# Kernel optimization log

Hardware: AMD Instinct MI355X
Metric: run time of the kernel (lower is better)

## Reference

```python
import jax, jax.numpy as jnp
import numpy as np

S, D, H, MLP = 2048, 1024, 16, 4096
DK = D // H
EPS = 1e-5  # torch LayerNorm default


def setup_inputs() -> dict:
    key = jax.random.key(0)
    ks = jax.random.split(key, 8)
    init = lambda k, shape, fan_in: jax.random.normal(k, shape, jnp.float32) * (fan_in ** -0.5)
    return {
        "x": jax.random.normal(ks[0], (S, D), jnp.float32),
        "wq": init(ks[1], (D, D), D), "bq": jnp.zeros((D,), jnp.float32),
        "wk": init(ks[2], (D, D), D), "bk": jnp.zeros((D,), jnp.float32),
        "wv": init(ks[3], (D, D), D), "bv": jnp.zeros((D,), jnp.float32),
        "wo": init(ks[4], (D, D), D), "bo": jnp.zeros((D,), jnp.float32),
        "w1": init(ks[5], (D, MLP), D), "b1": jnp.zeros((MLP,), jnp.float32),
        "w2": init(ks[6], (MLP, D), MLP), "b2": jnp.zeros((D,), jnp.float32),
        "ln1_g": jnp.ones((D,), jnp.float32), "ln1_b": jnp.zeros((D,), jnp.float32),
        "ln2_g": jnp.ones((D,), jnp.float32), "ln2_b": jnp.zeros((D,), jnp.float32),
    }


def _layernorm(x, g, b):
    m = jnp.mean(x, axis=-1, keepdims=True)
    v = jnp.var(x, axis=-1, keepdims=True)
    return (x - m) * jax.lax.rsqrt(v + EPS) * g + b


def reference(x, wq, bq, wk, bk, wv, bv, wo, bo, w1, b1, w2, b2, ln1_g, ln1_b, ln2_g, ln2_b):
    # --- residual 1: pre-LN multi-head self-attention ---
    h = _layernorm(x, ln1_g, ln1_b)
    q = (h @ wq + bq).reshape(S, H, DK).transpose(1, 0, 2)  # [H,S,DK]
    k = (h @ wk + bk).reshape(S, H, DK).transpose(1, 0, 2)
    v = (h @ wv + bv).reshape(S, H, DK).transpose(1, 0, 2)
    scores = jnp.einsum('hqd,hkd->hqk', q, k) / jnp.sqrt(jnp.float32(DK))  # [H,S,S]
    attn = jax.nn.softmax(scores, axis=-1)
    o = jnp.einsum('hqk,hkd->hqd', attn, v)  # [H,S,DK]
    # Faithful to original: x.contiguous().view(S, -1) is a raw reshape of the
    # [H,S,DK] buffer (no transpose back to [S,H,DK]).
    o = o.reshape(S, D)
    x = x + (o @ wo + bo)
    # --- residual 2: pre-LN GELU FFN ---
    h2 = _layernorm(x, ln2_g, ln2_b)
    f = jax.nn.gelu(h2 @ w1 + b1, approximate=False)  # torch nn.GELU = exact erf
    x = x + (f @ w2 + b2)
    return x
```

## Files before the change

### kernel.cpp

```cpp
#include <hip/hip_runtime.h>


constexpr int kS = 2048, kD = 1024, kH = 16, kDK = 64, kMLP = 4096;
constexpr float kEps = 1e-5f;

using u16 = unsigned short;
using u32 = unsigned int;
typedef float f32x4 __attribute__((ext_vector_type(4)));
typedef short bf16x8 __attribute__((ext_vector_type(8)));

__device__ __forceinline__ u16 f2b(float f) {
  u32 u = __builtin_bit_cast(u32, f);
  return (u16)((u + 0x7fffu + ((u >> 16) & 1u)) >> 16);
}

typedef const __attribute__((address_space(1))) u32* gas1;
typedef __attribute__((address_space(3))) u32* las3;
__device__ __forceinline__ void async16(const void* g, void* l) {
  __builtin_amdgcn_global_load_lds((gas1)g, (las3)l, 16, 0, 0);
}

__global__ __launch_bounds__(256)
void ln_kernel(const float* __restrict__ x, const float* __restrict__ g,
               const float* __restrict__ b, u16* __restrict__ out) {
  __shared__ float red[8];
  const int row = blockIdx.x, tid = threadIdx.x;
  const float4 v = *(const float4*)(x + (size_t)row * kD + tid * 4);
  float s = v.x + v.y + v.z + v.w;
  float ss = v.x * v.x + v.y * v.y + v.z * v.z + v.w * v.w;
#pragma unroll
  for (int d = 1; d < 64; d <<= 1) { s += __shfl_xor(s, d); ss += __shfl_xor(ss, d); }
  if ((tid & 63) == 0) { red[tid >> 6] = s; red[4 + (tid >> 6)] = ss; }
  __syncthreads();
  const float m = (red[0] + red[1] + red[2] + red[3]) * (1.f / kD);
  const float var = (red[4] + red[5] + red[6] + red[7]) * (1.f / kD) - m * m;
  const float r = rsqrtf(var + kEps);
  const float4 gv = *(const float4*)(g + tid * 4);
  const float4 bv = *(const float4*)(b + tid * 4);
  ushort4 o;
  o.x = f2b((v.x - m) * r * gv.x + bv.x);
  o.y = f2b((v.y - m) * r * gv.y + bv.y);
  o.z = f2b((v.z - m) * r * gv.z + bv.z);
  o.w = f2b((v.w - m) * r * gv.w + bv.w);
  *(ushort4*)(out + (size_t)row * kD + tid * 4) = o;
}

__global__ __launch_bounds__(256)
void transpose_cvt(const float* __restrict__ in, u16* __restrict__ out, int R, int C) {
  __shared__ float tile[32][33];
  const int c0 = blockIdx.x * 32, r0 = blockIdx.y * 32;
  const int x = threadIdx.x, y = threadIdx.y;
#pragma unroll
  for (int i = 0; i < 4; ++i)
    tile[y + i * 8][x] = in[(size_t)(r0 + y + i * 8) * C + c0 + x];
  __syncthreads();
#pragma unroll
  for (int i = 0; i < 4; ++i)
    out[(size_t)(c0 + y + i * 8) * R + r0 + x] = f2b(tile[x][y + i * 8]);
}

__global__ void concat_bias(const float* __restrict__ bq, const float* __restrict__ bk,
                            const float* __restrict__ bv, float* __restrict__ out) {
  int i = blockIdx.x * 256 + threadIdx.x;
  out[i] = i < kD ? bq[i] : (i < 2 * kD ? bk[i - kD] : bv[i - 2 * kD]);
}

__global__ __launch_bounds__(256)
void vtrans(const u16* __restrict__ qkv, u16* __restrict__ vt) {
  __shared__ u16 t[64][72];
  const int s0 = blockIdx.x * 64, h = blockIdx.y, tid = threadIdx.x;
#pragma unroll
  for (int r = 0; r < 2; ++r) {
    int chunk = r * 256 + tid, row = chunk >> 3, col = (chunk & 7) * 8;
    uint4 v = *(const uint4*)(qkv + (size_t)(s0 + row) * 3072 + 2 * kD + h * 64 + col);
    *(uint4*)(&t[row][col]) = v;
  }
  __syncthreads();
#pragma unroll
  for (int r = 0; r < 2; ++r) {
    int chunk = r * 256 + tid, drow = chunk >> 3, scol = (chunk & 7) * 8;
    u16 tmp[8];
#pragma unroll
    for (int j = 0; j < 8; ++j) tmp[j] = t[scol + j][drow];
    *(uint4*)(vt + (size_t)h * 64 * kS + (size_t)drow * kS + s0 + scol) = *(uint4*)tmp;
  }
}

template <int EPI>
__global__ __launch_bounds__(256, 2)
void gemm_bt(const u16* __restrict__ A, const u16* __restrict__ Bt,
             const float* __restrict__ bias, void* __restrict__ Cout,
             int N, int K, int Ksub) {
  constexpr int BM = 128, BN = 128, BK = 32;
  constexpr int MT = 4, NT = 4;
  __shared__ u16 As[BM * BK];
  __shared__ u16 Bs[BN * BK];
  const int tid = threadIdx.x;
  const int w = tid >> 6, l = tid & 63;
  const int wm = w >> 1, wn = w & 1;
  const int row0 = blockIdx.y * BM, col0 = blockIdx.x * BN;
  const int koff = blockIdx.z * Ksub;

  const int sc = ((l & 3) ^ ((l >> 3) & 3)) * 8;
  const u16* Ag = A + (size_t)(row0 + w * 16 + (l >> 2)) * K + koff + sc;
  const u16* Bg = Bt + (size_t)(col0 + w * 16 + (l >> 2)) * K + koff + sc;
  u16* AsW = As + w * 512;
  u16* BsW = Bs + w * 512;

  f32x4 acc[MT][NT] = {};
  const int q = l >> 4;

  for (int kt = 0; kt < Ksub; kt += BK) {
#pragma unroll
    for (int r = 0; r < 2; ++r) async16(Ag + (size_t)r * 64 * K + kt, AsW + r * 2048);
#pragma unroll
    for (int r = 0; r < 2; ++r) async16(Bg + (size_t)r * 64 * K + kt, BsW + r * 2048);
    __syncthreads();
    bf16x8 af[MT], bfr[NT];
#pragma unroll
    for (int i = 0; i < MT; ++i) {
      const int ra = wm * 64 + i * 16 + (l & 15);
      af[i] = *(const bf16x8*)(As + ra * 32 + (q ^ ((ra >> 1) & 3)) * 8);
    }
#pragma unroll
    for (int j = 0; j < NT; ++j) {
      const int rb = wn * 64 + j * 16 + (l & 15);
      bfr[j] = *(const bf16x8*)(Bs + rb * 32 + (q ^ ((rb >> 1) & 3)) * 8);
    }
#pragma unroll
    for (int i = 0; i < MT; ++i)
#pragma unroll
      for (int j = 0; j < NT; ++j)
        acc[i][j] = __builtin_amdgcn_mfma_f32_16x16x32_bf16(af[i], bfr[j], acc[i][j], 0, 0, 0);
    __syncthreads();
  }

  float* Pf = nullptr;
  if constexpr (EPI == 3)
    Pf = (float*)Cout + (size_t)blockIdx.z * gridDim.y * BM * N;
#pragma unroll
  for (int i = 0; i < MT; ++i) {
    const int row = row0 + wm * 64 + i * 16 + ((l >> 4) << 2);
#pragma unroll
    for (int j = 0; j < NT; ++j) {
      const int col = col0 + wn * 64 + j * 16 + (l & 15);
      float bb = 0.f;
      if constexpr (EPI != 3) bb = bias[col];
#pragma unroll
      for (int r = 0; r < 4; ++r) {
        const size_t idx = (size_t)(row + r) * N + col;
        float v = acc[i][j][r] + bb;
        if constexpr (EPI == 0) {
          ((u16*)Cout)[idx] = f2b(v);
        } else if constexpr (EPI == 1) {
          ((u16*)Cout)[idx] = f2b(0.5f * v * (1.f + erff(v * 0.7071067811865475f)));
        } else {
          Pf[idx] = v;
        }
      }
    }
  }
}

template <int KS>
__global__ __launch_bounds__(256)
void reduce_add(const float* __restrict__ parts, const float* __restrict__ bias,
                const float* __restrict__ res, float* __restrict__ out,
                int N, size_t strideMN) {
  const size_t b = ((size_t)blockIdx.x * 256 + threadIdx.x) * 4;
  float4 a = *(const float4*)(res + b);
  const float4 bv = *(const float4*)(bias + (b & (size_t)(N - 1)));
  a.x += bv.x; a.y += bv.y; a.z += bv.z; a.w += bv.w;
#pragma unroll
  for (int s = 0; s < KS; ++s) {
    const float4 p = *(const float4*)(parts + s * strideMN + b);
    a.x += p.x; a.y += p.y; a.z += p.z; a.w += p.w;
  }
  *(float4*)(out + b) = a;
}

__global__ __launch_bounds__(256)
void flash_attn(const u16* __restrict__ qkv, const u16* __restrict__ vt,
                float* __restrict__ Op, float* __restrict__ Ml) {
  constexpr int LP = 140;
  __shared__ u16 PsQ[4 * 16 * LP];
  __shared__ u16 Ks[128 * 64];
  __shared__ u16 Vs[64 * 128];
  const int tid = threadIdx.x, w = tid >> 6, l = tid & 63;
  const int h = blockIdx.y, q0 = blockIdx.x * 64, z = blockIdx.z;
  const int kt0 = z * (kS / 2);
  const int q = l >> 4;

  const u16* Qg = qkv + h * 64;
  const u16* Kg = qkv + kD + h * 64;
  const u16* Vg = vt + (size_t)h * 64 * kS;

  {
    const int r8 = l >> 3, c = (l & 7) ^ r8;
#pragma unroll
    for (int p = 0; p < 2; ++p) {
      const int row = (p * 4 + w) * 8 + r8;
      async16(Qg + (size_t)(q0 + row) * 3072 + c * 8, PsQ + (p * 4 + w) * 512);
    }
  }
  __syncthreads();
  bf16x8 qa[2];
  const int rq = w * 16 + (l & 15);
#pragma unroll
  for (int kq = 0; kq < 2; ++kq)
    qa[kq] = *(const bf16x8*)(PsQ + rq * 64 + ((kq * 4 + q) ^ (l & 7)) * 8);
  u16* Ps = PsQ + w * 16 * LP;

  f32x4 oacc[4] = {};
  float mi[4], li[4];
#pragma unroll
  for (int r = 0; r < 4; ++r) { mi[r] = -1e30f; li[r] = 0.f; }

  for (int it = 0; it < 8; ++it) {
    __syncthreads();
    const int kt = kt0 + it * 128;
    {
      const int r8 = l >> 3, c = (l & 7) ^ r8;
#pragma unroll
      for (int p = 0; p < 4; ++p) {
        const int row = (p * 4 + w) * 8 + r8;
        async16(Kg + (size_t)(kt + row) * 3072 + c * 8, Ks + (p * 4 + w) * 512);
      }
    }
    {
#pragma unroll
      for (int p = 0; p < 4; ++p) {
        const int row = (p * 4 + w) * 4 + (l >> 4);
        const int c = (l & 15) ^ (row & 7);
        async16(Vg + (size_t)row * kS + kt + c * 8, Vs + (p * 4 + w) * 512);
      }
    }
    __syncthreads();

    f32x4 s[8];
#pragma unroll
    for (int n = 0; n < 8; ++n) {
      const int rk = n * 16 + (l & 15);
      f32x4 zz = {};
      bf16x8 kb0 = *(const bf16x8*)(Ks + rk * 64 + ((0 + q) ^ (rk & 7)) * 8);
      bf16x8 kb1 = *(const bf16x8*)(Ks + rk * 64 + ((4 + q) ^ (rk & 7)) * 8);
      zz = __builtin_amdgcn_mfma_f32_16x16x32_bf16(qa[0], kb0, zz, 0, 0, 0);
      zz = __builtin_amdgcn_mfma_f32_16x16x32_bf16(qa[1], kb1, zz, 0, 0, 0);
      s[n] = zz;
    }
    float alpha[4];
#pragma unroll
    for (int r = 0; r < 4; ++r) {
      float m = -1e30f;
#pragma unroll
      for (int n = 0; n < 8; ++n) m = fmaxf(m, s[n][r]);
#pragma unroll
      for (int d = 1; d < 16; d <<= 1) m = fmaxf(m, __shfl_xor(m, d));
      m *= 0.125f;
      float mn = fmaxf(mi[r], m);
      alpha[r] = __expf(mi[r] - mn);
      mi[r] = mn;
      li[r] *= alpha[r];
    }
#pragma unroll
    for (int n = 0; n < 4; ++n)
#pragma unroll
      for (int r = 0; r < 4; ++r) oacc[n][r] *= alpha[r];
    float rs[4] = {0.f, 0.f, 0.f, 0.f};
#pragma unroll
    for (int n = 0; n < 8; ++n)
#pragma unroll
      for (int r = 0; r < 4; ++r) {
        float pv = __expf(s[n][r] * 0.125f - mi[r]);
        rs[r] += pv;
        Ps[((l >> 4) * 4 + r) * LP + n * 16 + (l & 15)] = f2b(pv);
      }
#pragma unroll
    for (int r = 0; r < 4; ++r) {
      float t = rs[r];
#pragma unroll
      for (int d = 1; d < 16; d <<= 1) t += __shfl_xor(t, d);
      li[r] += t;
    }
    bf16x8 pa[4];
#pragma unroll
    for (int ks = 0; ks < 4; ++ks)
      pa[ks] = *(const bf16x8*)(&Ps[(l & 15) * LP + ks * 32 + q * 8]);
#pragma unroll
    for (int n = 0; n < 4; ++n) {
      const int rv = n * 16 + (l & 15);
#pragma unroll
      for (int ks = 0; ks < 4; ++ks) {
        bf16x8 vb = *(const bf16x8*)(Vs + rv * 128 + ((ks * 4 + q) ^ (rv & 7)) * 8);
        oacc[n] = __builtin_amdgcn_mfma_f32_16x16x32_bf16(pa[ks], vb, oacc[n], 0, 0, 0);
      }
    }
  }

#pragma unroll
  for (int r = 0; r < 4; ++r) {
    const int srow = q0 + w * 16 + (l >> 4) * 4 + r;
    const size_t rowIdx = (size_t)(z * kH + h) * kS + srow;
    if ((l & 15) == 0) { Ml[rowIdx * 2] = mi[r]; Ml[rowIdx * 2 + 1] = li[r]; }
#pragma unroll
    for (int n = 0; n < 4; ++n)
      Op[rowIdx * kDK + n * 16 + (l & 15)] = oacc[n][r];
  }
}

__global__ __launch_bounds__(256)
void flash_combine(const float* __restrict__ Op, const float* __restrict__ Ml,
                   u16* __restrict__ og) {
  constexpr size_t HS = (size_t)kH * kS;
  constexpr size_t ZO = HS * kDK;
  const int t = blockIdx.x * 256 + threadIdx.x;
  const int d4 = (t & 15) * 4;
  const size_t row = (size_t)(t >> 4);
  const float m0 = Ml[row * 2], l0 = Ml[row * 2 + 1];
  const float m1 = Ml[(HS + row) * 2], l1 = Ml[(HS + row) * 2 + 1];
  const float m = fmaxf(m0, m1);
  const float w0 = __expf(m0 - m), w1 = __expf(m1 - m);
  const float inv = 1.f / (w0 * l0 + w1 * l1);
  const float4 a = *(const float4*)(Op + row * kDK + d4);
  const float4 b = *(const float4*)(Op + ZO + row * kDK + d4);
  ushort4 o;
  o.x = f2b((w0 * a.x + w1 * b.x) * inv);
  o.y = f2b((w0 * a.y + w1 * b.y) * inv);
  o.z = f2b((w0 * a.z + w1 * b.z) * inv);
  o.w = f2b((w0 * a.w + w1 * b.w) * inv);
  *(ushort4*)(og + row * kDK + d4) = o;
}

extern "C" void kernel_launch(void* const* d_in, const int* in_sizes, int n_in,
                              void* d_out, int out_size, void* d_ws, size_t ws_size,
                              hipStream_t stream) {
  const float* x = (const float*)d_in[0];
  const float* wq = (const float*)d_in[1];
  const float* bq = (const float*)d_in[2];
  const float* wk = (const float*)d_in[3];
  const float* bk = (const float*)d_in[4];
  const float* wv = (const float*)d_in[5];
  const float* bv = (const float*)d_in[6];
  const float* wo = (const float*)d_in[7];
  const float* bo = (const float*)d_in[8];
  const float* w1 = (const float*)d_in[9];
  const float* b1 = (const float*)d_in[10];
  const float* w2 = (const float*)d_in[11];
  const float* b2 = (const float*)d_in[12];
  const float* ln1g = (const float*)d_in[13];
  const float* ln1b = (const float*)d_in[14];
  const float* ln2g = (const float*)d_in[15];
  const float* ln2b = (const float*)d_in[16];
  float* out = (float*)d_out;

  char* p = (char*)d_ws;
  auto alloc = [&](size_t bytes) { void* q = (void*)p; p += (bytes + 255) & ~(size_t)255; return q; };
  u16* h1 = (u16*)alloc((size_t)kS * kD * 2);
  u16* wqkvt = (u16*)alloc((size_t)3 * kD * kD * 2);
  u16* qkv = (u16*)alloc((size_t)kS * 3 * kD * 2);
  u16* vt = (u16*)alloc((size_t)kH * kDK * kS * 2);
  u16* og = (u16*)alloc((size_t)kS * kD * 2);
  u16* wot = (u16*)alloc((size_t)kD * kD * 2);
  u16* h2 = (u16*)alloc((size_t)kS * kD * 2);
  u16* w1t = (u16*)alloc((size_t)kD * kMLP * 2);
  float* bqkv = (float*)alloc((size_t)3 * kD * 4);
  float* x2 = (float*)alloc((size_t)kS * kD * 4);
  u16* fbuf = (u16*)alloc((size_t)kS * kMLP * 2);
  u16* w2t = (u16*)alloc((size_t)kMLP * kD * 2);
  float* part = (float*)d_ws;
  float* Op = x2;
  float* Ml = Op + (size_t)2 * kH * kS * kDK;
  const size_t strideMN = (size_t)kS * kD;

  dim3 tb(32, 8);
  transpose_cvt<<<dim3(kD / 32, kD / 32), tb, 0, stream>>>(wq, wqkvt, kD, kD);
  transpose_cvt<<<dim3(kD / 32, kD / 32), tb, 0, stream>>>(wk, wqkvt + kD * kD, kD, kD);
  transpose_cvt<<<dim3(kD / 32, kD / 32), tb, 0, stream>>>(wv, wqkvt + 2 * kD * kD, kD, kD);
  transpose_cvt<<<dim3(kD / 32, kD / 32), tb, 0, stream>>>(wo, wot, kD, kD);
  transpose_cvt<<<dim3(kMLP / 32, kD / 32), tb, 0, stream>>>(w1, w1t, kD, kMLP);
  transpose_cvt<<<dim3(kD / 32, kMLP / 32), tb, 0, stream>>>(w2, w2t, kMLP, kD);
  concat_bias<<<dim3(12), dim3(256), 0, stream>>>(bq, bk, bv, bqkv);

  ln_kernel<<<dim3(kS), dim3(256), 0, stream>>>(x, ln1g, ln1b, h1);
  gemm_bt<0><<<dim3(3 * kD / 128, kS / 128, 1), dim3(256), 0, stream>>>(
      h1, wqkvt, bqkv, qkv, 3 * kD, kD, kD);
  vtrans<<<dim3(kS / 64, kH), dim3(256), 0, stream>>>(qkv, vt);
  flash_attn<<<dim3(kS / 64, kH, 2), dim3(256), 0, stream>>>(qkv, vt, Op, Ml);
  flash_combine<<<dim3(kH * kS * 16 / 256), dim3(256), 0, stream>>>(Op, Ml, og);
  gemm_bt<3><<<dim3(kD / 128, kS / 128, 2), dim3(256), 0, stream>>>(
      og, wot, nullptr, part, kD, kD, kD / 2);
  reduce_add<2><<<dim3(kS * kD / 4 / 256), dim3(256), 0, stream>>>(
      part, bo, x, x2, kD, strideMN);
  ln_kernel<<<dim3(kS), dim3(256), 0, stream>>>(x2, ln2g, ln2b, h2);
  gemm_bt<1><<<dim3(kMLP / 128, kS / 128, 1), dim3(256), 0, stream>>>(
      h2, w1t, b1, fbuf, kMLP, kD, kD);
  gemm_bt<3><<<dim3(kD / 128, kS / 128, 4), dim3(256), 0, stream>>>(
      fbuf, w2t, nullptr, part, kD, kMLP, kMLP / 4);
  reduce_add<4><<<dim3(kS * kD / 4 / 256), dim3(256), 0, stream>>>(
      part, b2, x2, out, kD, strideMN);
}
```

Baseline: 332.2 us.

## Replace LDS-staged GEMM with direct global-to-register double-buffered MFMA loads

```diff
diff --git a/kernel.cpp b/kernel.cpp
--- a/kernel.cpp
+++ b/kernel.cpp
@@ -87,63 +87,71 @@
 }
 
 template <int EPI>
-__global__ __launch_bounds__(256, 2)
-void gemm_bt(const u16* __restrict__ A, const u16* __restrict__ Bt,
+__global__ __launch_bounds__(256)
+void gemm_rd(const u16* __restrict__ A, const u16* __restrict__ Bt,
              const float* __restrict__ bias, void* __restrict__ Cout,
              int N, int K, int Ksub) {
-  constexpr int BM = 128, BN = 128, BK = 32;
-  constexpr int MT = 4, NT = 4;
-  __shared__ u16 As[BM * BK];
-  __shared__ u16 Bs[BN * BK];
-  const int tid = threadIdx.x;
-  const int w = tid >> 6, l = tid & 63;
+  const int tid = threadIdx.x, w = tid >> 6, l = tid & 63;
   const int wm = w >> 1, wn = w & 1;
-  const int row0 = blockIdx.y * BM, col0 = blockIdx.x * BN;
+  const int row0 = blockIdx.y * 128 + wm * 64;
+  const int col0 = blockIdx.x * 128 + wn * 64;
   const int koff = blockIdx.z * Ksub;
 
-  const int sc = ((l & 3) ^ ((l >> 3) & 3)) * 8;
-  const u16* Ag = A + (size_t)(row0 + w * 16 + (l >> 2)) * K + koff + sc;
-  const u16* Bg = Bt + (size_t)(col0 + w * 16 + (l >> 2)) * K + koff + sc;
-  u16* AsW = As + w * 512;
-  u16* BsW = Bs + w * 512;
-
-  f32x4 acc[MT][NT] = {};
-  const int q = l >> 4;
-
-  for (int kt = 0; kt < Ksub; kt += BK) {
-#pragma unroll
-    for (int r = 0; r < 2; ++r) async16(Ag + (size_t)r * 64 * K + kt, AsW + r * 2048);
-#pragma unroll
-    for (int r = 0; r < 2; ++r) async16(Bg + (size_t)r * 64 * K + kt, BsW + r * 2048);
-    __syncthreads();
-    bf16x8 af[MT], bfr[NT];
-#pragma unroll
-    for (int i = 0; i < MT; ++i) {
-      const int ra = wm * 64 + i * 16 + (l & 15);
-      af[i] = *(const bf16x8*)(As + ra * 32 + (q ^ ((ra >> 1) & 3)) * 8);
-    }
-#pragma unroll
-    for (int j = 0; j < NT; ++j) {
-      const int rb = wn * 64 + j * 16 + (l & 15);
-      bfr[j] = *(const bf16x8*)(Bs + rb * 32 + (q ^ ((rb >> 1) & 3)) * 8);
-    }
-#pragma unroll
-    for (int i = 0; i < MT; ++i)
-#pragma unroll
-      for (int j = 0; j < NT; ++j)
-        acc[i][j] = __builtin_amdgcn_mfma_f32_16x16x32_bf16(af[i], bfr[j], acc[i][j], 0, 0, 0);
-    __syncthreads();
-  }
+  const u16* Ab = A + (size_t)(row0 + (l & 15)) * K + koff + (l >> 4) * 8;
+  const u16* Bb = Bt + (size_t)(col0 + (l & 15)) * K + koff + (l >> 4) * 8;
+
+  f32x4 acc[4][4] = {};
+  bf16x8 a0[4], b0[4], a1[4], b1[4];
+
+  auto ld0 = [&](int kt) {
+#pragma unroll
+    for (int i = 0; i < 4; ++i) a0[i] = *(const bf16x8*)(Ab + (size_t)i * 16 * K + kt);
+#pragma unroll
+    for (int j = 0; j < 4; ++j) b0[j] = *(const bf16x8*)(Bb + (size_t)j * 16 * K + kt);
+  };
+  auto ld1 = [&](int kt) {
+#pragma unroll
+    for (int i = 0; i < 4; ++i) a1[i] = *(const bf16x8*)(Ab + (size_t)i * 16 * K + kt);
+#pragma unroll
+    for (int j = 0; j < 4; ++j) b1[j] = *(const bf16x8*)(Bb + (size_t)j * 16 * K + kt);
+  };
+  auto fma0 = [&]() {
+#pragma unroll
+    for (int i = 0; i < 4; ++i)
+#pragma unroll
+      for (int j = 0; j < 4; ++j)
+        acc[i][j] = __builtin_amdgcn_mfma_f32_16x16x32_bf16(a0[i], b0[j], acc[i][j], 0, 0, 0);
+  };
+  auto fma1 = [&]() {
+#pragma unroll
+    for (int i = 0; i < 4; ++i)
+#pragma unroll
+      for (int j = 0; j < 4; ++j)
+        acc[i][j] = __builtin_amdgcn_mfma_f32_16x16x32_bf16(a1[i], b1[j], acc[i][j], 0, 0, 0);
+  };
+
+  const int steps = Ksub / 32;
+  ld0(0);
+  int s = 0;
+  for (; s + 2 < steps; s += 2) {
+    ld1((s + 1) * 32);
+    fma0();
+    ld0((s + 2) * 32);
+    fma1();
+  }
+  ld1((s + 1) * 32);
+  fma0();
+  fma1();
 
   float* Pf = nullptr;
   if constexpr (EPI == 3)
-    Pf = (float*)Cout + (size_t)blockIdx.z * gridDim.y * BM * N;
-#pragma unroll
-  for (int i = 0; i < MT; ++i) {
-    const int row = row0 + wm * 64 + i * 16 + ((l >> 4) << 2);
-#pragma unroll
-    for (int j = 0; j < NT; ++j) {
-      const int col = col0 + wn * 64 + j * 16 + (l & 15);
+    Pf = (float*)Cout + (size_t)blockIdx.z * gridDim.y * 128 * N;
+#pragma unroll
+  for (int i = 0; i < 4; ++i) {
+    const int row = row0 + i * 16 + ((l >> 4) << 2);
+#pragma unroll
+    for (int j = 0; j < 4; ++j) {
+      const int col = col0 + j * 16 + (l & 15);
       float bb = 0.f;
       if constexpr (EPI != 3) bb = bias[col];
 #pragma unroll
@@ -382,19 +390,19 @@
   concat_bias<<<dim3(12), dim3(256), 0, stream>>>(bq, bk, bv, bqkv);
 
   ln_kernel<<<dim3(kS), dim3(256), 0, stream>>>(x, ln1g, ln1b, h1);
-  gemm_bt<0><<<dim3(3 * kD / 128, kS / 128, 1), dim3(256), 0, stream>>>(
+  gemm_rd<0><<<dim3(3 * kD / 128, kS / 128, 1), dim3(256), 0, stream>>>(
       h1, wqkvt, bqkv, qkv, 3 * kD, kD, kD);
   vtrans<<<dim3(kS / 64, kH), dim3(256), 0, stream>>>(qkv, vt);
   flash_attn<<<dim3(kS / 64, kH, 2), dim3(256), 0, stream>>>(qkv, vt, Op, Ml);
   flash_combine<<<dim3(kH * kS * 16 / 256), dim3(256), 0, stream>>>(Op, Ml, og);
-  gemm_bt<3><<<dim3(kD / 128, kS / 128, 2), dim3(256), 0, stream>>>(
+  gemm_rd<3><<<dim3(kD / 128, kS / 128, 2), dim3(256), 0, stream>>>(
       og, wot, nullptr, part, kD, kD, kD / 2);
   reduce_add<2><<<dim3(kS * kD / 4 / 256), dim3(256), 0, stream>>>(
       part, bo, x, x2, kD, strideMN);
   ln_kernel<<<dim3(kS), dim3(256), 0, stream>>>(x2, ln2g, ln2b, h2);
-  gemm_bt<1><<<dim3(kMLP / 128, kS / 128, 1), dim3(256), 0, stream>>>(
+  gemm_rd<1><<<dim3(kMLP / 128, kS / 128, 1), dim3(256), 0, stream>>>(
       h2, w1t, b1, fbuf, kMLP, kD, kD);
-  gemm_bt<3><<<dim3(kD / 128, kS / 128, 4), dim3(256), 0, stream>>>(
+  gemm_rd<3><<<dim3(kD / 128, kS / 128, 4), dim3(256), 0, stream>>>(
       fbuf, w2t, nullptr, part, kD, kMLP, kMLP / 4);
   reduce_add<4><<<dim3(kS * kD / 4 / 256), dim3(256), 0, stream>>>(
       part, b2, x2, out, kD, strideMN);
```

Result: slower. 440.2 us (+32.5%).
